# Kernel optimization log

Measured on AMD Instinct MI355X. Metric: run time of the kernel, lower is better.

Reference implementation:

```python
import jax, jax.numpy as jnp
import numpy as np

B, NN, F, H = 8, 1024, 256, 8
D = F // H
SCALE = D ** -0.5


def setup_inputs() -> dict:
    key = jax.random.key(0)
    ks = jax.random.split(key, 12)
    s = 0.02
    inp = {
        'ndata': jax.random.normal(ks[0], (B, NN, F), jnp.float32),
        'N': NN,
        'attn_bias': jax.random.normal(ks[1], (B, NN, NN, H), jnp.float32),
        'attn_mask': jax.random.randint(ks[2], (B, NN, NN), 0, 2).astype(bool),
        'Wq': jax.random.normal(ks[3], (F, F), jnp.float32) * s,
        'bq': jnp.zeros((F,), jnp.float32),
        'Wk': jax.random.normal(ks[4], (F, F), jnp.float32) * s,
        'bk': jnp.zeros((F,), jnp.float32),
        'Wv': jax.random.normal(ks[5], (F, F), jnp.float32) * s,
        'bv': jnp.zeros((F,), jnp.float32),
        'Wo': jax.random.normal(ks[6], (F, F), jnp.float32) * s,
        'bo': jnp.zeros((F,), jnp.float32),
    }
    return inp


def reference(ndata, N, attn_bias, attn_mask, Wq, bq, Wk, bk, Wv, bv, Wo, bo):
    b, n, f = ndata.shape
    # QKV projections (torch nn.Linear: x @ W.T + b), split heads
    q = (ndata @ Wq.T + bq).reshape(b, n, H, D) * SCALE
    k = (ndata @ Wk.T + bk).reshape(b, n, H, D)
    v = (ndata @ Wv.T + bv).reshape(b, n, H, D)
    # scores: (b, q, k, h) matching torch layout after its transposes
    scores = jnp.einsum('bqhd,bkhd->bqkh', q, k)
    scores = scores + attn_bias  # additive bias
    # original code force-unmasks column 0 so every row has a valid entry
    mask = attn_mask.at[:, :, 0].set(False)
    scores = jnp.where(mask[..., None], -jnp.inf, scores)
    attn = jax.nn.softmax(scores, axis=2)  # softmax over keys
    out = jnp.einsum('bqkh,bkhd->bqhd', attn, v).reshape(b, n, f)
    return out @ Wo.T + bo
```

## Files before the change

### kernel.cpp

```cpp
#include <hip/hip_runtime.h>
#include <hip/hip_bf16.h>

typedef __attribute__((ext_vector_type(8))) short short8;
typedef __attribute__((ext_vector_type(4))) float f32x4;

#define MFMA16(a,b,c) __builtin_amdgcn_mfma_f32_16x16x32_bf16((a),(b),(c),0,0,0)

static __device__ __forceinline__ unsigned int f2bf(float f){
    unsigned int u = __float_as_uint(f);
    u += 0x7FFFu + ((u >> 16) & 1u);
    return u >> 16;
}

static __device__ __forceinline__ short8 pack8(float4 a, float4 b){
    short8 r;
    r[0]=(short)f2bf(a.x); r[1]=(short)f2bf(a.y);
    r[2]=(short)f2bf(a.z); r[3]=(short)f2bf(a.w);
    r[4]=(short)f2bf(b.x); r[5]=(short)f2bf(b.y);
    r[6]=(short)f2bf(b.z); r[7]=(short)f2bf(b.w);
    return r;
}

__global__ __launch_bounds__(256) void mask_prep_k(
    const unsigned int* __restrict__ m, unsigned int* __restrict__ bmout)
{
    __shared__ int any_hi;
    const int tid  = threadIdx.x;
    const int lane = tid & 63;
    const unsigned int gbase = blockIdx.x*256u + tid;
    if (tid == 0) any_hi = 0;

    unsigned int wv[8]; unsigned int acc = 0;
    #pragma unroll
    for (int it = 0; it < 8; ++it){
        wv[it] = m[it*262144u + gbase];
        acc |= wv[it];
    }
    __syncthreads();
    if (acc & 0xFFFFFF00u) atomicOr(&any_hi, 1);
    __syncthreads();

    if (any_hi == 0){
        for (int it = 0; it < 32; ++it){
            unsigned int idx = it*262144u + gbase;
            unsigned int v = m[idx];
            unsigned long long bal = __ballot(v != 0u);
            if (lane == 0)
                *(unsigned long long*)(bmout + (idx >> 5)) = bal;
        }
    } else {
        #pragma unroll
        for (int it = 0; it < 8; ++it){
            unsigned int idx = it*262144u + gbase;
            unsigned int v = wv[it];
            unsigned int nib = (v | (v>>7) | (v>>14) | (v>>21)) & 0xFu;
            unsigned int x = nib << ((lane & 7)*4);
            x |= (unsigned int)__shfl_xor((int)x, 1);
            x |= (unsigned int)__shfl_xor((int)x, 2);
            x |= (unsigned int)__shfl_xor((int)x, 4);
            if ((lane & 7) == 0)
                bmout[idx >> 3] = x;
        }
    }
}

__global__ __launch_bounds__(256) void qkv_proj_k(
    const float* __restrict__ nd,
    const float* __restrict__ Wqp, const float* __restrict__ bqp,
    const float* __restrict__ Wkp, const float* __restrict__ bkp,
    const float* __restrict__ Wvp, const float* __restrict__ bvp,
    unsigned short* __restrict__ qout, unsigned short* __restrict__ kout,
    unsigned short* __restrict__ vtout)
{
    __shared__ __align__(16) unsigned short xl[64*264];
    const int tid  = threadIdx.x;
    const int bi   = blockIdx.x;
    const int kind = bi >> 7;
    const int R0   = (bi & 127) * 64;
    const int b    = R0 >> 10;
    const int n0   = R0 & 1023;

    #pragma unroll
    for (int it = 0; it < 16; ++it){
        int f4 = it*256 + tid;
        int r = f4 >> 6, c4 = f4 & 63;
        float4 v = *(const float4*)(nd + (size_t)(R0+r)*256 + c4*4);
        unsigned int lo = f2bf(v.x) | (f2bf(v.y) << 16);
        unsigned int hi = f2bf(v.z) | (f2bf(v.w) << 16);
        *(uint2*)&xl[r*264 + c4*4] = make_uint2(lo, hi);
    }
    __syncthreads();

    const int lane = tid & 63;
    const int w  = tid >> 6;
    const int ln = lane & 15;
    const int g  = lane >> 4;
    const int ow = w * 64;

    f32x4 acc[4][4];
    #pragma unroll
    for (int a=0;a<4;++a){
        #pragma unroll
        for (int c=0;c<4;++c) acc[a][c] = (f32x4){0.f,0.f,0.f,0.f};
    }

    if (kind < 2){
        const float* W  = kind ? Wkp : Wqp;
        const float* bb = kind ? bkp : bqp;
        unsigned short* op = kind ? kout : qout;
        const float scl = kind ? 1.0f : 0.17677669529663687f;
        for (int kk = 0; kk < 8; ++kk){
            short8 wf[4], xf[4];
            #pragma unroll
            for (int ot=0; ot<4; ++ot){
                const float* wp = W + (size_t)(ow + ot*16 + ln)*256 + kk*32 + g*8;
                wf[ot] = pack8(*(const float4*)wp, *(const float4*)(wp+4));
            }
            #pragma unroll
            for (int nt=0; nt<4; ++nt)
                xf[nt] = *(const short8*)&xl[(nt*16+ln)*264 + kk*32 + g*8];
            #pragma unroll
            for (int ot=0; ot<4; ++ot){
                #pragma unroll
                for (int nt=0; nt<4; ++nt)
                    acc[ot][nt] = MFMA16(wf[ot], xf[nt], acc[ot][nt]);
            }
        }
        #pragma unroll
        for (int ot=0; ot<4; ++ot){
            int o0 = ow + ot*16 + g*4;
            int h = o0 >> 5, d0 = o0 & 31;
            float4 b4 = *(const float4*)(bb + o0);
            #pragma unroll
            for (int nt=0; nt<4; ++nt){
                int n = n0 + nt*16 + ln;
                unsigned int lo = f2bf((acc[ot][nt][0]+b4.x)*scl) | (f2bf((acc[ot][nt][1]+b4.y)*scl)<<16);
                unsigned int hi = f2bf((acc[ot][nt][2]+b4.z)*scl) | (f2bf((acc[ot][nt][3]+b4.w)*scl)<<16);
                *(uint2*)(op + ((size_t)(b*8+h)*1024 + n)*32 + d0) = make_uint2(lo,hi);
            }
        }
    } else {
        for (int kk = 0; kk < 8; ++kk){
            short8 wf[4], xf[4];
            #pragma unroll
            for (int ot=0; ot<4; ++ot){
                const float* wp = Wvp + (size_t)(ow + ot*16 + ln)*256 + kk*32 + g*8;
                wf[ot] = pack8(*(const float4*)wp, *(const float4*)(wp+4));
            }
            #pragma unroll
            for (int nt=0; nt<4; ++nt)
                xf[nt] = *(const short8*)&xl[(nt*16+ln)*264 + kk*32 + g*8];
            #pragma unroll
            for (int nt=0; nt<4; ++nt){
                #pragma unroll
                for (int ot=0; ot<4; ++ot)
                    acc[nt][ot] = MFMA16(xf[nt], wf[ot], acc[nt][ot]);
            }
        }
        #pragma unroll
        for (int nt=0; nt<4; ++nt){
            int nb = n0 + nt*16 + g*4;
            #pragma unroll
            for (int ot=0; ot<4; ++ot){
                int o = ow + ot*16 + ln;
                int h = o >> 5, d = o & 31;
                float bvv = bvp[o];
                unsigned int lo = f2bf(acc[nt][ot][0]+bvv) | (f2bf(acc[nt][ot][1]+bvv)<<16);
                unsigned int hi = f2bf(acc[nt][ot][2]+bvv) | (f2bf(acc[nt][ot][3]+bvv)<<16);
                *(uint2*)(vtout + ((size_t)(b*8+h)*32 + d)*1024 + nb) = make_uint2(lo,hi);
            }
        }
    }
}

__global__ __launch_bounds__(256, 4) void attn_k(
    const unsigned short* __restrict__ qbuf, const unsigned short* __restrict__ kbuf,
    const unsigned short* __restrict__ vtbuf, const float* __restrict__ bias,
    const unsigned int* __restrict__ bm, unsigned short* __restrict__ ab)
{
    __shared__ float bs[2048];
    const int tid  = threadIdx.x;
    const int bi   = blockIdx.x;
    const int hh   = bi & 1;
    const int qt   = (bi >> 1) & 63;
    const int b    = bi >> 7;
    const int q0   = qt * 16;
    const int lane = tid & 63;
    const int w    = tid >> 6;
    const int ln   = lane & 15;
    const int g    = lane >> 4;
    const int h    = hh*4 + w;

    const short8 qf = *(const short8*)(qbuf + ((size_t)(b*8+h)*1024 + q0 + ln)*32 + g*8);

    const int kperm = ((ln >> 2) << 3) + (ln & 3);
    const unsigned short* kp = kbuf  + ((size_t)(b*8+h)*1024 + kperm)*32 + g*8;
    const unsigned short* vp = vtbuf + ((size_t)(b*8+h)*32 + ln)*1024 + g*8;
    const unsigned int* bmp  = bm + (size_t)(b*1024 + q0 + ln)*32;

    const int qt0 = tid >> 5;
    const int kk0 = tid & 31;
    const float* bgp0 = bias + ((size_t)(b*1024 + q0 + qt0)*1024 + kk0)*8 + hh*4;
    const float* bgp1 = bgp0 + 65536;
    const int kx  = kk0 ^ qt0;
    const int w0i = qt0*32 + kx;
    const int w1i = w0i + 256;

    const int base_rg = w*512 + ln*32 + g*8;
    const int lnx = ln & 7;

    f32x4 acc0 = (f32x4){0.f,0.f,0.f,0.f};
    f32x4 acc1 = (f32x4){0.f,0.f,0.f,0.f};
    float lsum = 0.f;
    const f32x4 z4 = {0.f,0.f,0.f,0.f};

    float4 br0, br1;
    short8 kA0, kA1, vA0, vA1, kB0, kB1, vB0, vB1;
    unsigned int bmA, bmB;

#define LOAD_BIAS(cc) do { int c_=(cc); \
    br0 = *(const float4*)(bgp0 + c_*256); \
    br1 = *(const float4*)(bgp1 + c_*256); } while(0)

#define STAGE() do { \
    bs[w0i       ] = br0.x; bs[w0i +  512] = br0.y; \
    bs[w0i + 1024] = br0.z; bs[w0i + 1536] = br0.w; \
    bs[w1i       ] = br1.x; bs[w1i +  512] = br1.y; \
    bs[w1i + 1024] = br1.z; bs[w1i + 1536] = br1.w; } while(0)

#define LOAD_KVM(S, cc) do { int c_=(cc); \
    k##S##0 = *(const short8*)(kp + c_*1024); \
    k##S##1 = *(const short8*)(kp + c_*1024 + 128); \
    v##S##0 = *(const short8*)(vp + c_*32); \
    v##S##1 = *(const short8*)(vp + c_*32 + 16*1024); \
    bm##S   = bmp[c_]; } while(0)

#define COMPUTE(S) do { \
    unsigned int mb_ = bm##S >> (g*8); \
    f32x4 s0 = MFMA16(k##S##0, qf, z4); \
    f32x4 s1 = MFMA16(k##S##1, qf, z4); \
    float e0 = __expf(((mb_>>0)&1u) ? -1e30f : s0[0] + bs[base_rg + (0^lnx)]); \
    float e1 = __expf(((mb_>>1)&1u) ? -1e30f : s0[1] + bs[base_rg + (1^lnx)]); \
    float e2 = __expf(((mb_>>2)&1u) ? -1e30f : s0[2] + bs[base_rg + (2^lnx)]); \
    float e3 = __expf(((mb_>>3)&1u) ? -1e30f : s0[3] + bs[base_rg + (3^lnx)]); \
    float e4 = __expf(((mb_>>4)&1u) ? -1e30f : s1[0] + bs[base_rg + (4^lnx)]); \
    float e5 = __expf(((mb_>>5)&1u) ? -1e30f : s1[1] + bs[base_rg + (5^lnx)]); \
    float e6 = __expf(((mb_>>6)&1u) ? -1e30f : s1[2] + bs[base_rg + (6^lnx)]); \
    float e7 = __expf(((mb_>>7)&1u) ? -1e30f : s1[3] + bs[base_rg + (7^lnx)]); \
    lsum += ((e0+e1)+(e2+e3)) + ((e4+e5)+(e6+e7)); \
    int4 pw_ = make_int4( \
        (int)(f2bf(e0) | (f2bf(e1)<<16)), (int)(f2bf(e2) | (f2bf(e3)<<16)), \
        (int)(f2bf(e4) | (f2bf(e5)<<16)), (int)(f2bf(e6) | (f2bf(e7)<<16))); \
    short8 pf_ = *(short8*)&pw_; \
    acc0 = MFMA16(v##S##0, pf_, acc0); \
    acc1 = MFMA16(v##S##1, pf_, acc1); } while(0)

    LOAD_BIAS(0);
    LOAD_KVM(A, 0);
    bmA &= ~1u;

    #pragma unroll 1
    for (int c = 0; c < 32; c += 2){
        STAGE();
        LOAD_BIAS(c + 1);
        __syncthreads();
        LOAD_KVM(B, c + 1);
        COMPUTE(A);
        __syncthreads();
        STAGE();
        if (c + 2 < 32) LOAD_BIAS(c + 2);
        __syncthreads();
        if (c + 2 < 32) LOAD_KVM(A, c + 2);
        COMPUTE(B);
        __syncthreads();
    }

    float ps = lsum;
    ps += __shfl_xor(ps, 16);
    ps += __shfl_xor(ps, 32);
    float inv = 1.0f / ps;
    {
        size_t orow = ((size_t)(b*1024 + q0 + ln))*256 + h*32;
        unsigned int lo0 = f2bf(acc0[0]*inv) | (f2bf(acc0[1]*inv)<<16);
        unsigned int hi0 = f2bf(acc0[2]*inv) | (f2bf(acc0[3]*inv)<<16);
        *(uint2*)(ab + orow + g*4) = make_uint2(lo0,hi0);
        unsigned int lo1 = f2bf(acc1[0]*inv) | (f2bf(acc1[1]*inv)<<16);
        unsigned int hi1 = f2bf(acc1[2]*inv) | (f2bf(acc1[3]*inv)<<16);
        *(uint2*)(ab + orow + 16 + g*4) = make_uint2(lo1,hi1);
    }
#undef LOAD_BIAS
#undef STAGE
#undef LOAD_KVM
#undef COMPUTE
}

__global__ __launch_bounds__(256) void oproj_k(
    const unsigned short* __restrict__ ab, const float* __restrict__ Wop,
    const float* __restrict__ bop, float* __restrict__ out)
{
    __shared__ __align__(16) unsigned short al[32*264];
    const int tid = threadIdx.x;
    const int R0 = blockIdx.x * 32;
    #pragma unroll
    for (int it=0; it<4; ++it){
        int f8 = it*256 + tid;
        int r = f8 >> 5, c8 = f8 & 31;
        *(short8*)&al[r*264 + c8*8] = *(const short8*)(ab + (size_t)(R0+r)*256 + c8*8);
    }
    __syncthreads();
    const int lane = tid & 63;
    const int w = tid >> 6, ln = lane & 15, g = lane >> 4;
    const int ow = w*64;
    f32x4 acc[4][2];
    #pragma unroll
    for (int a=0;a<4;++a){ acc[a][0]=(f32x4){0.f,0.f,0.f,0.f}; acc[a][1]=(f32x4){0.f,0.f,0.f,0.f}; }
    for (int kk=0;kk<8;++kk){
        short8 wf[4], xf[2];
        #pragma unroll
        for (int ot=0;ot<4;++ot){
            const float* wp = Wop + (size_t)(ow+ot*16+ln)*256 + kk*32 + g*8;
            wf[ot] = pack8(*(const float4*)wp, *(const float4*)(wp+4));
        }
        #pragma unroll
        for (int nt=0;nt<2;++nt)
            xf[nt] = *(const short8*)&al[(nt*16+ln)*264 + kk*32 + g*8];
        #pragma unroll
        for (int ot=0;ot<4;++ot){
            #pragma unroll
            for (int nt=0;nt<2;++nt)
                acc[ot][nt] = MFMA16(wf[ot], xf[nt], acc[ot][nt]);
        }
    }
    #pragma unroll
    for (int ot=0;ot<4;++ot){
        int o0 = ow + ot*16 + g*4;
        float4 b4 = *(const float4*)(bop + o0);
        #pragma unroll
        for (int nt=0;nt<2;++nt){
            int n = R0 + nt*16 + ln;
            float4 res;
            res.x = acc[ot][nt][0] + b4.x;
            res.y = acc[ot][nt][1] + b4.y;
            res.z = acc[ot][nt][2] + b4.z;
            res.w = acc[ot][nt][3] + b4.w;
            *(float4*)(out + (size_t)n*256 + o0) = res;
        }
    }
}

extern "C" void kernel_launch(void* const* d_in, const int* in_sizes, int n_in,
                              void* d_out, int out_size, void* d_ws, size_t ws_size,
                              hipStream_t stream)
{
    (void)in_sizes; (void)n_in; (void)out_size; (void)ws_size;
    const float* nd   = (const float*)d_in[0];
    const float* bias = (const float*)d_in[2];
    const int* mask   = (const int*)d_in[3];
    const float* Wq = (const float*)d_in[4];
    const float* bq = (const float*)d_in[5];
    const float* Wk = (const float*)d_in[6];
    const float* bk = (const float*)d_in[7];
    const float* Wv = (const float*)d_in[8];
    const float* bv = (const float*)d_in[9];
    const float* Wo = (const float*)d_in[10];
    const float* bo = (const float*)d_in[11];
    float* out = (float*)d_out;

    const size_t ELEMS = (size_t)8*8*1024*32;
    unsigned short* qb  = (unsigned short*)d_ws;
    unsigned short* kb  = qb  + ELEMS;
    unsigned short* vtb = kb  + ELEMS;
    unsigned short* ab  = vtb + ELEMS;
    unsigned int* bmw   = (unsigned int*)(ab + ELEMS);

    mask_prep_k<<<1024, 256, 0, stream>>>((const unsigned int*)mask, bmw);
    qkv_proj_k<<<384, 256, 0, stream>>>(nd, Wq, bq, Wk, bk, Wv, bv, qb, kb, vtb);
    attn_k<<<1024, 256, 0, stream>>>(qb, kb, vtb, bias, bmw, ab);
    oproj_k<<<256, 256, 0, stream>>>(ab, Wo, bo, out);
}
```

Measured before the change: 170.3 us.

## Process all eight heads per attention block with full-row bias loads

The attention kernel now uses 512-thread blocks covering all 8 heads for a 16-query tile, so each bias row of 8 heads×keys is read contiguously as full float4 rows rather than split across two blocks by head half. Chunks double to 32 keys each with a single sync pair per iteration, and keys are loaded in natural order with lane shuffles rebuilding the P operand layout. V fragments are loaded inside the compute step instead of prefetched. This is meant to improve bias read coalescing and halve barrier count, at the cost of more shuffles, larger LDS use and possibly lower occupancy.

```diff
diff --git a/kernel.cpp b/kernel.cpp
--- a/kernel.cpp
+++ b/kernel.cpp
@@ -173,105 +173,117 @@
     }
 }
 
-__global__ __launch_bounds__(256, 4) void attn_k(
+__global__ __launch_bounds__(512, 4) void attn_k(
     const unsigned short* __restrict__ qbuf, const unsigned short* __restrict__ kbuf,
     const unsigned short* __restrict__ vtbuf, const float* __restrict__ bias,
     const unsigned int* __restrict__ bm, unsigned short* __restrict__ ab)
 {
-    __shared__ float bs[2048];
+    __shared__ float bs[8192];
     const int tid  = threadIdx.x;
     const int bi   = blockIdx.x;
-    const int hh   = bi & 1;
-    const int qt   = (bi >> 1) & 63;
-    const int b    = bi >> 7;
-    const int q0   = qt * 16;
+    const int b    = bi >> 6;
+    const int q0   = (bi & 63) * 16;
     const int lane = tid & 63;
     const int w    = tid >> 6;
     const int ln   = lane & 15;
     const int g    = lane >> 4;
-    const int h    = hh*4 + w;
-
-    const short8 qf = *(const short8*)(qbuf + ((size_t)(b*8+h)*1024 + q0 + ln)*32 + g*8);
-
-    const int kperm = ((ln >> 2) << 3) + (ln & 3);
-    const unsigned short* kp = kbuf  + ((size_t)(b*8+h)*1024 + kperm)*32 + g*8;
-    const unsigned short* vp = vtbuf + ((size_t)(b*8+h)*32 + ln)*1024 + g*8;
-    const unsigned int* bmp  = bm + (size_t)(b*1024 + q0 + ln)*32;
-
-    const int qt0 = tid >> 5;
-    const int kk0 = tid & 31;
-    const float* bgp0 = bias + ((size_t)(b*1024 + q0 + qt0)*1024 + kk0)*8 + hh*4;
-    const float* bgp1 = bgp0 + 65536;
-    const int kx  = kk0 ^ qt0;
-    const int w0i = qt0*32 + kx;
-    const int w1i = w0i + 256;
-
-    const int base_rg = w*512 + ln*32 + g*8;
-    const int lnx = ln & 7;
+
+    const short8 qf = *(const short8*)(qbuf + ((size_t)(b*8+w)*1024 + q0 + ln)*32 + g*8);
+
+    const int h2s  = lane & 1;
+    const int keys = lane >> 1;
+    const int ts   = keys >> 4;
+    const int rs   = keys & 3;
+    const int gs   = (keys >> 2) & 3;
+    const int base0 = (128*ts + 32*rs + 16*h2s + gs) * 16;
+    const int xrs   = (8*ts + 2*rs + h2s) & 15;
+    const int qxa   = (2*w)     ^ xrs;
+    const int qxb   = (2*w + 1) ^ xrs;
+
+    const float* bp0 = bias + ((size_t)(b*1024 + q0 + 2*w)*1024)*8 + lane*4;
+    const unsigned short* kp = kbuf  + ((size_t)(b*8+w)*1024 + ln)*32 + g*8;
+    const unsigned short* vp = vtbuf + ((size_t)(b*8+w)*32   + ln)*1024 + g*8;
+    const unsigned int*  bmp = bm + (size_t)(b*1024 + q0 + ln)*32;
 
     f32x4 acc0 = (f32x4){0.f,0.f,0.f,0.f};
     f32x4 acc1 = (f32x4){0.f,0.f,0.f,0.f};
     float lsum = 0.f;
     const f32x4 z4 = {0.f,0.f,0.f,0.f};
 
-    float4 br0, br1;
-    short8 kA0, kA1, vA0, vA1, kB0, kB1, vB0, vB1;
-    unsigned int bmA, bmB;
-
-#define LOAD_BIAS(cc) do { int c_=(cc); \
-    br0 = *(const float4*)(bgp0 + c_*256); \
-    br1 = *(const float4*)(bgp1 + c_*256); } while(0)
-
-#define STAGE() do { \
-    bs[w0i       ] = br0.x; bs[w0i +  512] = br0.y; \
-    bs[w0i + 1024] = br0.z; bs[w0i + 1536] = br0.w; \
-    bs[w1i       ] = br1.x; bs[w1i +  512] = br1.y; \
-    bs[w1i + 1024] = br1.z; bs[w1i + 1536] = br1.w; } while(0)
-
-#define LOAD_KVM(S, cc) do { int c_=(cc); \
-    k##S##0 = *(const short8*)(kp + c_*1024); \
-    k##S##1 = *(const short8*)(kp + c_*1024 + 128); \
-    v##S##0 = *(const short8*)(vp + c_*32); \
-    v##S##1 = *(const short8*)(vp + c_*32 + 16*1024); \
-    bm##S   = bmp[c_]; } while(0)
-
-#define COMPUTE(S) do { \
-    unsigned int mb_ = bm##S >> (g*8); \
-    f32x4 s0 = MFMA16(k##S##0, qf, z4); \
-    f32x4 s1 = MFMA16(k##S##1, qf, z4); \
-    float e0 = __expf(((mb_>>0)&1u) ? -1e30f : s0[0] + bs[base_rg + (0^lnx)]); \
-    float e1 = __expf(((mb_>>1)&1u) ? -1e30f : s0[1] + bs[base_rg + (1^lnx)]); \
-    float e2 = __expf(((mb_>>2)&1u) ? -1e30f : s0[2] + bs[base_rg + (2^lnx)]); \
-    float e3 = __expf(((mb_>>3)&1u) ? -1e30f : s0[3] + bs[base_rg + (3^lnx)]); \
-    float e4 = __expf(((mb_>>4)&1u) ? -1e30f : s1[0] + bs[base_rg + (4^lnx)]); \
-    float e5 = __expf(((mb_>>5)&1u) ? -1e30f : s1[1] + bs[base_rg + (5^lnx)]); \
-    float e6 = __expf(((mb_>>6)&1u) ? -1e30f : s1[2] + bs[base_rg + (6^lnx)]); \
-    float e7 = __expf(((mb_>>7)&1u) ? -1e30f : s1[3] + bs[base_rg + (7^lnx)]); \
-    lsum += ((e0+e1)+(e2+e3)) + ((e4+e5)+(e6+e7)); \
-    int4 pw_ = make_int4( \
-        (int)(f2bf(e0) | (f2bf(e1)<<16)), (int)(f2bf(e2) | (f2bf(e3)<<16)), \
-        (int)(f2bf(e4) | (f2bf(e5)<<16)), (int)(f2bf(e6) | (f2bf(e7)<<16))); \
+    float4 b00, b01, b10, b11;
+    short8 kn0, kn1, kn2, kn3;
+    unsigned int bm0, bm1;
+
+#define LOAD_ALL(cc) do { int c_ = (cc); \
+    b00 = *(const float4*)(bp0 + (size_t)c_*512); \
+    b01 = *(const float4*)(bp0 + (size_t)c_*512 + 256); \
+    b10 = *(const float4*)(bp0 + (size_t)c_*512 + 8192); \
+    b11 = *(const float4*)(bp0 + (size_t)c_*512 + 8192 + 256); \
+    kn0 = *(const short8*)(kp + c_*2048); \
+    kn1 = *(const short8*)(kp + c_*2048 + 512); \
+    kn2 = *(const short8*)(kp + c_*2048 + 1024); \
+    kn3 = *(const short8*)(kp + c_*2048 + 1536); \
+    bm0 = bmp[2*c_]; bm1 = bmp[2*c_+1]; } while(0)
+
+#define CHUNK_HALF(K0, K1, BMW, BOFF, VOFF) do { \
+    f32x4 s0 = MFMA16(K0, qf, z4); \
+    f32x4 s1 = MFMA16(K1, qf, z4); \
+    short8 vf0 = *(const short8*)(vp + (VOFF)); \
+    short8 vf1 = *(const short8*)(vp + (VOFF) + 16*1024); \
+    float pv[8]; \
+    _Pragma("unroll") for (int t=0; t<2; ++t){ \
+        _Pragma("unroll") for (int r=0; r<4; ++r){ \
+            int keyl = t*16 + g*4 + r; \
+            int bidx = (BOFF) + (t*128 + r*32 + w*4 + g)*16 + (ln ^ ((t*8 + r*2 + (w>>2)) & 15)); \
+            float sv = (t ? s1[r] : s0[r]) + bs[bidx]; \
+            sv = (((BMW) >> keyl) & 1u) ? -1e30f : sv; \
+            float p = __expf(sv); \
+            pv[t*4+r] = p; \
+            lsum += p; \
+        } \
+    } \
+    unsigned int A01 = f2bf(pv[0]) | (f2bf(pv[1])<<16); \
+    unsigned int A23 = f2bf(pv[2]) | (f2bf(pv[3])<<16); \
+    unsigned int B01 = f2bf(pv[4]) | (f2bf(pv[5])<<16); \
+    unsigned int B23 = f2bf(pv[6]) | (f2bf(pv[7])<<16); \
+    int s0l = (2*(g&1))*16 + ln; \
+    int s1l = s0l + 16; \
+    unsigned int a01  = (unsigned int)__shfl((int)A01, s0l); \
+    unsigned int a23  = (unsigned int)__shfl((int)A23, s0l); \
+    unsigned int c01  = (unsigned int)__shfl((int)B01, s0l); \
+    unsigned int c23  = (unsigned int)__shfl((int)B23, s0l); \
+    unsigned int a01b = (unsigned int)__shfl((int)A01, s1l); \
+    unsigned int a23b = (unsigned int)__shfl((int)A23, s1l); \
+    unsigned int c01b = (unsigned int)__shfl((int)B01, s1l); \
+    unsigned int c23b = (unsigned int)__shfl((int)B23, s1l); \
+    bool hi_ = (g >= 2); \
+    int4 pw_ = make_int4((int)(hi_ ? c01  : a01 ), (int)(hi_ ? c23  : a23 ), \
+                         (int)(hi_ ? c01b : a01b), (int)(hi_ ? c23b : a23b)); \
     short8 pf_ = *(short8*)&pw_; \
-    acc0 = MFMA16(v##S##0, pf_, acc0); \
-    acc1 = MFMA16(v##S##1, pf_, acc1); } while(0)
-
-    LOAD_BIAS(0);
-    LOAD_KVM(A, 0);
-    bmA &= ~1u;
+    acc0 = MFMA16(vf0, pf_, acc0); \
+    acc1 = MFMA16(vf1, pf_, acc1); } while(0)
+
+    LOAD_ALL(0);
+    bm0 &= ~1u;
 
     #pragma unroll 1
-    for (int c = 0; c < 32; c += 2){
-        STAGE();
-        LOAD_BIAS(c + 1);
+    for (int cc = 0; cc < 16; ++cc){
+        bs[base0       + qxa] = b00.x;  bs[base0 +  64 + qxa] = b00.y;
+        bs[base0 + 128 + qxa] = b00.z;  bs[base0 + 192 + qxa] = b00.w;
+        bs[base0       + qxb] = b10.x;  bs[base0 +  64 + qxb] = b10.y;
+        bs[base0 + 128 + qxb] = b10.z;  bs[base0 + 192 + qxb] = b10.w;
+        bs[4096 + base0       + qxa] = b01.x;  bs[4096 + base0 +  64 + qxa] = b01.y;
+        bs[4096 + base0 + 128 + qxa] = b01.z;  bs[4096 + base0 + 192 + qxa] = b01.w;
+        bs[4096 + base0       + qxb] = b11.x;  bs[4096 + base0 +  64 + qxb] = b11.y;
+        bs[4096 + base0 + 128 + qxb] = b11.z;  bs[4096 + base0 + 192 + qxb] = b11.w;
+
+        short8 ck0 = kn0, ck1 = kn1, ck2 = kn2, ck3 = kn3;
+        unsigned int cb0 = bm0, cb1 = bm1;
+        if (cc + 1 < 16) LOAD_ALL(cc + 1);
         __syncthreads();
-        LOAD_KVM(B, c + 1);
-        COMPUTE(A);
-        __syncthreads();
-        STAGE();
-        if (c + 2 < 32) LOAD_BIAS(c + 2);
-        __syncthreads();
-        if (c + 2 < 32) LOAD_KVM(A, c + 2);
-        COMPUTE(B);
+
+        CHUNK_HALF(ck0, ck1, cb0, 0,    cc*64);
+        CHUNK_HALF(ck2, ck3, cb1, 4096, cc*64 + 32);
         __syncthreads();
     }
 
@@ -280,18 +292,16 @@
     ps += __shfl_xor(ps, 32);
     float inv = 1.0f / ps;
     {
-        size_t orow = ((size_t)(b*1024 + q0 + ln))*256 + h*32;
+        int n = q0 + ln;
         unsigned int lo0 = f2bf(acc0[0]*inv) | (f2bf(acc0[1]*inv)<<16);
         unsigned int hi0 = f2bf(acc0[2]*inv) | (f2bf(acc0[3]*inv)<<16);
-        *(uint2*)(ab + orow + g*4) = make_uint2(lo0,hi0);
+        *(uint2*)(ab + ((size_t)(b*1024 + n))*256 + w*32 + g*4) = make_uint2(lo0,hi0);
         unsigned int lo1 = f2bf(acc1[0]*inv) | (f2bf(acc1[1]*inv)<<16);
         unsigned int hi1 = f2bf(acc1[2]*inv) | (f2bf(acc1[3]*inv)<<16);
-        *(uint2*)(ab + orow + 16 + g*4) = make_uint2(lo1,hi1);
-    }
-#undef LOAD_BIAS
-#undef STAGE
-#undef LOAD_KVM
-#undef COMPUTE
+        *(uint2*)(ab + ((size_t)(b*1024 + n))*256 + w*32 + 16 + g*4) = make_uint2(lo1,hi1);
+    }
+#undef LOAD_ALL
+#undef CHUNK_HALF
 }
 
 __global__ __launch_bounds__(256) void oproj_k(
@@ -375,6 +385,6 @@
 
     mask_prep_k<<<1024, 256, 0, stream>>>((const unsigned int*)mask, bmw);
     qkv_proj_k<<<384, 256, 0, stream>>>(nd, Wq, bq, Wk, bk, Wv, bv, qb, kb, vtb);
-    attn_k<<<1024, 256, 0, stream>>>(qb, kb, vtb, bias, bmw, ab);
+    attn_k<<<512, 512, 0, stream>>>(qb, kb, vtb, bias, bmw, ab);
     oproj_k<<<256, 256, 0, stream>>>(ab, Wo, bo, out);
 }
```

Measured after the change: 143.6 us. -15.7%, faster.

## Pre-transpose bias to bf16 head-major with mask folded in, drop attention LDS staging

Applied to the files above, without the earlier changes.

A new pre-pass reads the fp32 (b,q,k,h) bias and the mask, applies the mask as -1e30 (keeping key column 0 unmasked), converts to bf16 and writes a head-major (b,h,q,k) buffer. The attention kernel then loads its bias fragment straight from global memory as short8, which removes the LDS staging, the four barriers per iteration and the mask-bit handling. In exchange it adds a 128 MB bf16 intermediate that is written and read back, plus an extra kernel launch and a one-block mask-format detector. Bias precision also drops to bf16.

```diff
diff --git a/kernel.cpp b/kernel.cpp
--- a/kernel.cpp
+++ b/kernel.cpp
@@ -10,6 +10,10 @@
     unsigned int u = __float_as_uint(f);
     u += 0x7FFFu + ((u >> 16) & 1u);
     return u >> 16;
+}
+
+static __device__ __forceinline__ float bf2f(unsigned short s){
+    return __uint_as_float(((unsigned int)s) << 16);
 }
 
 static __device__ __forceinline__ short8 pack8(float4 a, float4 b){
@@ -21,46 +25,67 @@
     return r;
 }
 
-__global__ __launch_bounds__(256) void mask_prep_k(
-    const unsigned int* __restrict__ m, unsigned int* __restrict__ bmout)
-{
+__global__ void detect_mask_k(const int* __restrict__ m, int* __restrict__ flag){
     __shared__ int any_hi;
+    if (threadIdx.x == 0) any_hi = 0;
+    __syncthreads();
+    int acc = 0;
+    #pragma unroll
+    for (int it = 0; it < 16; ++it)
+        acc |= m[it*256 + threadIdx.x];
+    if (acc & 0xFFFFFF00) atomicOr(&any_hi, 1);
+    __syncthreads();
+    if (threadIdx.x == 0) *flag = any_hi;
+}
+
+__global__ __launch_bounds__(256) void bias_prep_k(
+    const float* __restrict__ bias, const unsigned int* __restrict__ mask,
+    const int* __restrict__ mflag, unsigned short* __restrict__ bbt)
+{
+    __shared__ unsigned short tl[8][1032];
+    __shared__ unsigned int mbits[32];
     const int tid  = threadIdx.x;
-    const int lane = tid & 63;
-    const unsigned int gbase = blockIdx.x*256u + tid;
-    if (tid == 0) any_hi = 0;
-
-    unsigned int wv[8]; unsigned int acc = 0;
-    #pragma unroll
-    for (int it = 0; it < 8; ++it){
-        wv[it] = m[it*262144u + gbase];
-        acc |= wv[it];
-    }
-    __syncthreads();
-    if (acc & 0xFFFFFF00u) atomicOr(&any_hi, 1);
-    __syncthreads();
-
-    if (any_hi == 0){
-        for (int it = 0; it < 32; ++it){
-            unsigned int idx = it*262144u + gbase;
-            unsigned int v = m[idx];
+    const int row  = blockIdx.x;
+    const int b    = row >> 10, q = row & 1023;
+    const int lane = tid & 63, wv = tid >> 6;
+
+    if (*mflag == 0){
+        #pragma unroll
+        for (int i = 0; i < 4; ++i){
+            unsigned int v = mask[(size_t)row*1024 + i*256 + tid];
             unsigned long long bal = __ballot(v != 0u);
             if (lane == 0)
-                *(unsigned long long*)(bmout + (idx >> 5)) = bal;
+                *(unsigned long long*)&mbits[(i*256 + wv*64) >> 5] = bal;
         }
     } else {
-        #pragma unroll
-        for (int it = 0; it < 8; ++it){
-            unsigned int idx = it*262144u + gbase;
-            unsigned int v = wv[it];
-            unsigned int nib = (v | (v>>7) | (v>>14) | (v>>21)) & 0xFu;
-            unsigned int x = nib << ((lane & 7)*4);
-            x |= (unsigned int)__shfl_xor((int)x, 1);
-            x |= (unsigned int)__shfl_xor((int)x, 2);
-            x |= (unsigned int)__shfl_xor((int)x, 4);
-            if ((lane & 7) == 0)
-                bmout[idx >> 3] = x;
-        }
+        unsigned int v = mask[(size_t)row*256 + tid];
+        unsigned int nib = (v | (v>>7) | (v>>14) | (v>>21)) & 0xFu;
+        unsigned int x = nib << ((lane & 7)*4);
+        x |= (unsigned int)__shfl_xor((int)x, 1);
+        x |= (unsigned int)__shfl_xor((int)x, 2);
+        x |= (unsigned int)__shfl_xor((int)x, 4);
+        if ((lane & 7) == 0) mbits[tid >> 3] = x;
+    }
+    __syncthreads();
+
+    const int h0 = (tid & 1) * 4;
+    #pragma unroll
+    for (int i = 0; i < 8; ++i){
+        float4 v = *(const float4*)(bias + (size_t)row*8192 + i*1024 + tid*4);
+        int k = i*128 + (tid >> 1);
+        bool msk = (((mbits[k>>5] >> (k&31)) & 1u) != 0u) && (k != 0);
+        if (msk){ v.x = -1e30f; v.y = -1e30f; v.z = -1e30f; v.w = -1e30f; }
+        tl[h0  ][k] = (unsigned short)f2bf(v.x);
+        tl[h0+1][k] = (unsigned short)f2bf(v.y);
+        tl[h0+2][k] = (unsigned short)f2bf(v.z);
+        tl[h0+3][k] = (unsigned short)f2bf(v.w);
+    }
+    __syncthreads();
+
+    #pragma unroll
+    for (int h = 0; h < 8; ++h){
+        uint2 d = *(const uint2*)&tl[h][tid*4];
+        *(uint2*)(bbt + ((size_t)(b*8+h)*1024 + q)*1024 + tid*4) = d;
     }
 }
 
@@ -173,15 +198,14 @@
     }
 }
 
-__global__ __launch_bounds__(256, 4) void attn_k(
+__global__ __launch_bounds__(256, 4) void attn2_k(
     const unsigned short* __restrict__ qbuf, const unsigned short* __restrict__ kbuf,
-    const unsigned short* __restrict__ vtbuf, const float* __restrict__ bias,
-    const unsigned int* __restrict__ bm, unsigned short* __restrict__ ab)
-{
-    __shared__ float bs[2048];
+    const unsigned short* __restrict__ vtbuf, const unsigned short* __restrict__ bbt,
+    unsigned short* __restrict__ ab)
+{
     const int tid  = threadIdx.x;
     const int bi   = blockIdx.x;
-    const int hh   = bi & 1;
+    const int hg   = bi & 1;
     const int qt   = (bi >> 1) & 63;
     const int b    = bi >> 7;
     const int q0   = qt * 16;
@@ -189,90 +213,54 @@
     const int w    = tid >> 6;
     const int ln   = lane & 15;
     const int g    = lane >> 4;
-    const int h    = hh*4 + w;
+    const int h    = hg*4 + w;
 
     const short8 qf = *(const short8*)(qbuf + ((size_t)(b*8+h)*1024 + q0 + ln)*32 + g*8);
-
     const int kperm = ((ln >> 2) << 3) + (ln & 3);
     const unsigned short* kp = kbuf  + ((size_t)(b*8+h)*1024 + kperm)*32 + g*8;
     const unsigned short* vp = vtbuf + ((size_t)(b*8+h)*32 + ln)*1024 + g*8;
-    const unsigned int* bmp  = bm + (size_t)(b*1024 + q0 + ln)*32;
-
-    const int qt0 = tid >> 5;
-    const int kk0 = tid & 31;
-    const float* bgp0 = bias + ((size_t)(b*1024 + q0 + qt0)*1024 + kk0)*8 + hh*4;
-    const float* bgp1 = bgp0 + 65536;
-    const int kx  = kk0 ^ qt0;
-    const int w0i = qt0*32 + kx;
-    const int w1i = w0i + 256;
-
-    const int base_rg = w*512 + ln*32 + g*8;
-    const int lnx = ln & 7;
+    const unsigned short* bp = bbt   + ((size_t)(b*8+h)*1024 + q0 + ln)*1024 + g*8;
 
     f32x4 acc0 = (f32x4){0.f,0.f,0.f,0.f};
     f32x4 acc1 = (f32x4){0.f,0.f,0.f,0.f};
     float lsum = 0.f;
     const f32x4 z4 = {0.f,0.f,0.f,0.f};
 
-    float4 br0, br1;
-    short8 kA0, kA1, vA0, vA1, kB0, kB1, vB0, vB1;
-    unsigned int bmA, bmB;
-
-#define LOAD_BIAS(cc) do { int c_=(cc); \
-    br0 = *(const float4*)(bgp0 + c_*256); \
-    br1 = *(const float4*)(bgp1 + c_*256); } while(0)
-
-#define STAGE() do { \
-    bs[w0i       ] = br0.x; bs[w0i +  512] = br0.y; \
-    bs[w0i + 1024] = br0.z; bs[w0i + 1536] = br0.w; \
-    bs[w1i       ] = br1.x; bs[w1i +  512] = br1.y; \
-    bs[w1i + 1024] = br1.z; bs[w1i + 1536] = br1.w; } while(0)
-
-#define LOAD_KVM(S, cc) do { int c_=(cc); \
-    k##S##0 = *(const short8*)(kp + c_*1024); \
-    k##S##1 = *(const short8*)(kp + c_*1024 + 128); \
-    v##S##0 = *(const short8*)(vp + c_*32); \
-    v##S##1 = *(const short8*)(vp + c_*32 + 16*1024); \
-    bm##S   = bmp[c_]; } while(0)
-
-#define COMPUTE(S) do { \
-    unsigned int mb_ = bm##S >> (g*8); \
-    f32x4 s0 = MFMA16(k##S##0, qf, z4); \
-    f32x4 s1 = MFMA16(k##S##1, qf, z4); \
-    float e0 = __expf(((mb_>>0)&1u) ? -1e30f : s0[0] + bs[base_rg + (0^lnx)]); \
-    float e1 = __expf(((mb_>>1)&1u) ? -1e30f : s0[1] + bs[base_rg + (1^lnx)]); \
-    float e2 = __expf(((mb_>>2)&1u) ? -1e30f : s0[2] + bs[base_rg + (2^lnx)]); \
-    float e3 = __expf(((mb_>>3)&1u) ? -1e30f : s0[3] + bs[base_rg + (3^lnx)]); \
-    float e4 = __expf(((mb_>>4)&1u) ? -1e30f : s1[0] + bs[base_rg + (4^lnx)]); \
-    float e5 = __expf(((mb_>>5)&1u) ? -1e30f : s1[1] + bs[base_rg + (5^lnx)]); \
-    float e6 = __expf(((mb_>>6)&1u) ? -1e30f : s1[2] + bs[base_rg + (6^lnx)]); \
-    float e7 = __expf(((mb_>>7)&1u) ? -1e30f : s1[3] + bs[base_rg + (7^lnx)]); \
+    short8 k0A,k1A,v0A,v1A,bbA, k0B,k1B,v0B,v1B,bbB;
+
+#define LOADC(S, cc) do { int c_ = (cc); \
+    k0##S = *(const short8*)(kp + c_*1024); \
+    k1##S = *(const short8*)(kp + c_*1024 + 128); \
+    v0##S = *(const short8*)(vp + c_*32); \
+    v1##S = *(const short8*)(vp + c_*32 + 16*1024); \
+    bb##S = *(const short8*)(bp + c_*32); } while(0)
+
+#define COMPC(S) do { \
+    f32x4 s0 = MFMA16(k0##S, qf, z4); \
+    f32x4 s1 = MFMA16(k1##S, qf, z4); \
+    float e0 = __expf(s0[0] + bf2f((unsigned short)bb##S[0])); \
+    float e1 = __expf(s0[1] + bf2f((unsigned short)bb##S[1])); \
+    float e2 = __expf(s0[2] + bf2f((unsigned short)bb##S[2])); \
+    float e3 = __expf(s0[3] + bf2f((unsigned short)bb##S[3])); \
+    float e4 = __expf(s1[0] + bf2f((unsigned short)bb##S[4])); \
+    float e5 = __expf(s1[1] + bf2f((unsigned short)bb##S[5])); \
+    float e6 = __expf(s1[2] + bf2f((unsigned short)bb##S[6])); \
+    float e7 = __expf(s1[3] + bf2f((unsigned short)bb##S[7])); \
     lsum += ((e0+e1)+(e2+e3)) + ((e4+e5)+(e6+e7)); \
     int4 pw_ = make_int4( \
         (int)(f2bf(e0) | (f2bf(e1)<<16)), (int)(f2bf(e2) | (f2bf(e3)<<16)), \
         (int)(f2bf(e4) | (f2bf(e5)<<16)), (int)(f2bf(e6) | (f2bf(e7)<<16))); \
     short8 pf_ = *(short8*)&pw_; \
-    acc0 = MFMA16(v##S##0, pf_, acc0); \
-    acc1 = MFMA16(v##S##1, pf_, acc1); } while(0)
-
-    LOAD_BIAS(0);
-    LOAD_KVM(A, 0);
-    bmA &= ~1u;
-
+    acc0 = MFMA16(v0##S, pf_, acc0); \
+    acc1 = MFMA16(v1##S, pf_, acc1); } while(0)
+
+    LOADC(A, 0);
     #pragma unroll 1
     for (int c = 0; c < 32; c += 2){
-        STAGE();
-        LOAD_BIAS(c + 1);
-        __syncthreads();
-        LOAD_KVM(B, c + 1);
-        COMPUTE(A);
-        __syncthreads();
-        STAGE();
-        if (c + 2 < 32) LOAD_BIAS(c + 2);
-        __syncthreads();
-        if (c + 2 < 32) LOAD_KVM(A, c + 2);
-        COMPUTE(B);
-        __syncthreads();
+        LOADC(B, c + 1);
+        COMPC(A);
+        if (c + 2 < 32) LOADC(A, c + 2);
+        COMPC(B);
     }
 
     float ps = lsum;
@@ -288,10 +276,8 @@
         unsigned int hi1 = f2bf(acc1[2]*inv) | (f2bf(acc1[3]*inv)<<16);
         *(uint2*)(ab + orow + 16 + g*4) = make_uint2(lo1,hi1);
     }
-#undef LOAD_BIAS
-#undef STAGE
-#undef LOAD_KVM
-#undef COMPUTE
+#undef LOADC
+#undef COMPC
 }
 
 __global__ __launch_bounds__(256) void oproj_k(
@@ -371,10 +357,12 @@
     unsigned short* kb  = qb  + ELEMS;
     unsigned short* vtb = kb  + ELEMS;
     unsigned short* ab  = vtb + ELEMS;
-    unsigned int* bmw   = (unsigned int*)(ab + ELEMS);
-
-    mask_prep_k<<<1024, 256, 0, stream>>>((const unsigned int*)mask, bmw);
+    unsigned short* bbt = ab  + ELEMS;
+    int* mflag          = (int*)(bbt + (size_t)8*8*1024*1024);
+
+    detect_mask_k<<<1, 256, 0, stream>>>(mask, mflag);
     qkv_proj_k<<<384, 256, 0, stream>>>(nd, Wq, bq, Wk, bk, Wv, bv, qb, kb, vtb);
-    attn_k<<<1024, 256, 0, stream>>>(qb, kb, vtb, bias, bmw, ab);
+    bias_prep_k<<<8192, 256, 0, stream>>>(bias, (const unsigned int*)mask, mflag, bbt);
+    attn2_k<<<1024, 256, 0, stream>>>(qb, kb, vtb, bbt, ab);
     oproj_k<<<256, 256, 0, stream>>>(ab, Wo, bo, out);
 }
```

After: 188.5 us. 10.7% more time.

## Process two heads per wave and read bias directly without LDS staging

Applied to the files above, without the earlier changes.

Rewrites the attention kernel so each wave handles two heads for a 16-query tile, and a block covers all eight heads. Bias values are loaded straight from global memory as float2 pairs per key instead of being staged through shared memory, which removes the four barriers per iteration. Masking is applied after the exponential by zeroing. The trade-off is more registers per thread, half as many blocks, a lower occupancy target, and less-vectorised strided bias loads.

```diff
diff --git a/kernel.cpp b/kernel.cpp
--- a/kernel.cpp
+++ b/kernel.cpp
@@ -173,125 +173,138 @@
     }
 }
 
-__global__ __launch_bounds__(256, 4) void attn_k(
+__global__ __launch_bounds__(256, 2) void attn3_k(
     const unsigned short* __restrict__ qbuf, const unsigned short* __restrict__ kbuf,
     const unsigned short* __restrict__ vtbuf, const float* __restrict__ bias,
     const unsigned int* __restrict__ bm, unsigned short* __restrict__ ab)
 {
-    __shared__ float bs[2048];
     const int tid  = threadIdx.x;
     const int bi   = blockIdx.x;
-    const int hh   = bi & 1;
-    const int qt   = (bi >> 1) & 63;
-    const int b    = bi >> 7;
-    const int q0   = qt * 16;
+    const int b    = bi >> 6;
+    const int q0   = (bi & 63) * 16;
     const int lane = tid & 63;
     const int w    = tid >> 6;
     const int ln   = lane & 15;
     const int g    = lane >> 4;
-    const int h    = hh*4 + w;
-
-    const short8 qf = *(const short8*)(qbuf + ((size_t)(b*8+h)*1024 + q0 + ln)*32 + g*8);
+    const int h0   = 2*w, h1 = 2*w + 1;
+
+    const short8 qf0 = *(const short8*)(qbuf + ((size_t)(b*8+h0)*1024 + q0 + ln)*32 + g*8);
+    const short8 qf1 = *(const short8*)(qbuf + ((size_t)(b*8+h1)*1024 + q0 + ln)*32 + g*8);
 
     const int kperm = ((ln >> 2) << 3) + (ln & 3);
-    const unsigned short* kp = kbuf  + ((size_t)(b*8+h)*1024 + kperm)*32 + g*8;
-    const unsigned short* vp = vtbuf + ((size_t)(b*8+h)*32 + ln)*1024 + g*8;
-    const unsigned int* bmp  = bm + (size_t)(b*1024 + q0 + ln)*32;
-
-    const int qt0 = tid >> 5;
-    const int kk0 = tid & 31;
-    const float* bgp0 = bias + ((size_t)(b*1024 + q0 + qt0)*1024 + kk0)*8 + hh*4;
-    const float* bgp1 = bgp0 + 65536;
-    const int kx  = kk0 ^ qt0;
-    const int w0i = qt0*32 + kx;
-    const int w1i = w0i + 256;
-
-    const int base_rg = w*512 + ln*32 + g*8;
-    const int lnx = ln & 7;
-
-    f32x4 acc0 = (f32x4){0.f,0.f,0.f,0.f};
-    f32x4 acc1 = (f32x4){0.f,0.f,0.f,0.f};
-    float lsum = 0.f;
+    const unsigned short* kpA = kbuf + ((size_t)(b*8+h0)*1024 + kperm)*32 + g*8;
+    const unsigned short* kpB = kbuf + ((size_t)(b*8+h1)*1024 + kperm)*32 + g*8;
+    const unsigned short* vpA = vtbuf + ((size_t)(b*8+h0)*32 + ln)*1024 + g*8;
+    const unsigned short* vpB = vtbuf + ((size_t)(b*8+h1)*32 + ln)*1024 + g*8;
+    const float* bp = bias + (((size_t)(b*1024 + q0 + ln)*1024) + 8*g)*8 + h0;
+    const unsigned int* bmp = bm + (size_t)(b*1024 + q0 + ln)*32;
+
+    f32x4 acc00 = (f32x4){0.f,0.f,0.f,0.f};
+    f32x4 acc01 = (f32x4){0.f,0.f,0.f,0.f};
+    f32x4 acc10 = (f32x4){0.f,0.f,0.f,0.f};
+    f32x4 acc11 = (f32x4){0.f,0.f,0.f,0.f};
+    float lsum0 = 0.f, lsum1 = 0.f;
     const f32x4 z4 = {0.f,0.f,0.f,0.f};
 
-    float4 br0, br1;
-    short8 kA0, kA1, vA0, vA1, kB0, kB1, vB0, vB1;
+    short8 k0A,k1A,k2A,k3A, v0A,v1A,v2A,v3A;
+    short8 k0B,k1B,k2B,k3B, v0B,v1B,v2B,v3B;
+    float2 bb0A,bb1A,bb2A,bb3A,bb4A,bb5A,bb6A,bb7A;
+    float2 bb0B,bb1B,bb2B,bb3B,bb4B,bb5B,bb6B,bb7B;
     unsigned int bmA, bmB;
 
-#define LOAD_BIAS(cc) do { int c_=(cc); \
-    br0 = *(const float4*)(bgp0 + c_*256); \
-    br1 = *(const float4*)(bgp1 + c_*256); } while(0)
-
-#define STAGE() do { \
-    bs[w0i       ] = br0.x; bs[w0i +  512] = br0.y; \
-    bs[w0i + 1024] = br0.z; bs[w0i + 1536] = br0.w; \
-    bs[w1i       ] = br1.x; bs[w1i +  512] = br1.y; \
-    bs[w1i + 1024] = br1.z; bs[w1i + 1536] = br1.w; } while(0)
-
-#define LOAD_KVM(S, cc) do { int c_=(cc); \
-    k##S##0 = *(const short8*)(kp + c_*1024); \
-    k##S##1 = *(const short8*)(kp + c_*1024 + 128); \
-    v##S##0 = *(const short8*)(vp + c_*32); \
-    v##S##1 = *(const short8*)(vp + c_*32 + 16*1024); \
-    bm##S   = bmp[c_]; } while(0)
-
-#define COMPUTE(S) do { \
+#define LOADC(S, cc) do { int c_ = (cc); \
+    k0##S = *(const short8*)(kpA + c_*1024); \
+    k1##S = *(const short8*)(kpA + c_*1024 + 128); \
+    k2##S = *(const short8*)(kpB + c_*1024); \
+    k3##S = *(const short8*)(kpB + c_*1024 + 128); \
+    v0##S = *(const short8*)(vpA + c_*32); \
+    v1##S = *(const short8*)(vpA + c_*32 + 16*1024); \
+    v2##S = *(const short8*)(vpB + c_*32); \
+    v3##S = *(const short8*)(vpB + c_*32 + 16*1024); \
+    bb0##S = *(const float2*)(bp + (size_t)(c_*32+0)*8); \
+    bb1##S = *(const float2*)(bp + (size_t)(c_*32+1)*8); \
+    bb2##S = *(const float2*)(bp + (size_t)(c_*32+2)*8); \
+    bb3##S = *(const float2*)(bp + (size_t)(c_*32+3)*8); \
+    bb4##S = *(const float2*)(bp + (size_t)(c_*32+4)*8); \
+    bb5##S = *(const float2*)(bp + (size_t)(c_*32+5)*8); \
+    bb6##S = *(const float2*)(bp + (size_t)(c_*32+6)*8); \
+    bb7##S = *(const float2*)(bp + (size_t)(c_*32+7)*8); \
+    bm##S = bmp[c_]; } while(0)
+
+#define COMPC(S) do { \
     unsigned int mb_ = bm##S >> (g*8); \
-    f32x4 s0 = MFMA16(k##S##0, qf, z4); \
-    f32x4 s1 = MFMA16(k##S##1, qf, z4); \
-    float e0 = __expf(((mb_>>0)&1u) ? -1e30f : s0[0] + bs[base_rg + (0^lnx)]); \
-    float e1 = __expf(((mb_>>1)&1u) ? -1e30f : s0[1] + bs[base_rg + (1^lnx)]); \
-    float e2 = __expf(((mb_>>2)&1u) ? -1e30f : s0[2] + bs[base_rg + (2^lnx)]); \
-    float e3 = __expf(((mb_>>3)&1u) ? -1e30f : s0[3] + bs[base_rg + (3^lnx)]); \
-    float e4 = __expf(((mb_>>4)&1u) ? -1e30f : s1[0] + bs[base_rg + (4^lnx)]); \
-    float e5 = __expf(((mb_>>5)&1u) ? -1e30f : s1[1] + bs[base_rg + (5^lnx)]); \
-    float e6 = __expf(((mb_>>6)&1u) ? -1e30f : s1[2] + bs[base_rg + (6^lnx)]); \
-    float e7 = __expf(((mb_>>7)&1u) ? -1e30f : s1[3] + bs[base_rg + (7^lnx)]); \
-    lsum += ((e0+e1)+(e2+e3)) + ((e4+e5)+(e6+e7)); \
-    int4 pw_ = make_int4( \
+    f32x4 s0 = MFMA16(k0##S, qf0, z4); \
+    f32x4 s1 = MFMA16(k1##S, qf0, z4); \
+    f32x4 s2 = MFMA16(k2##S, qf1, z4); \
+    f32x4 s3 = MFMA16(k3##S, qf1, z4); \
+    float e0 = __expf(s0[0] + bb0##S.x); e0 = ((mb_>>0)&1u) ? 0.f : e0; \
+    float e1 = __expf(s0[1] + bb1##S.x); e1 = ((mb_>>1)&1u) ? 0.f : e1; \
+    float e2 = __expf(s0[2] + bb2##S.x); e2 = ((mb_>>2)&1u) ? 0.f : e2; \
+    float e3 = __expf(s0[3] + bb3##S.x); e3 = ((mb_>>3)&1u) ? 0.f : e3; \
+    float e4 = __expf(s1[0] + bb4##S.x); e4 = ((mb_>>4)&1u) ? 0.f : e4; \
+    float e5 = __expf(s1[1] + bb5##S.x); e5 = ((mb_>>5)&1u) ? 0.f : e5; \
+    float e6 = __expf(s1[2] + bb6##S.x); e6 = ((mb_>>6)&1u) ? 0.f : e6; \
+    float e7 = __expf(s1[3] + bb7##S.x); e7 = ((mb_>>7)&1u) ? 0.f : e7; \
+    float f0 = __expf(s2[0] + bb0##S.y); f0 = ((mb_>>0)&1u) ? 0.f : f0; \
+    float f1 = __expf(s2[1] + bb1##S.y); f1 = ((mb_>>1)&1u) ? 0.f : f1; \
+    float f2 = __expf(s2[2] + bb2##S.y); f2 = ((mb_>>2)&1u) ? 0.f : f2; \
+    float f3 = __expf(s2[3] + bb3##S.y); f3 = ((mb_>>3)&1u) ? 0.f : f3; \
+    float f4 = __expf(s3[0] + bb4##S.y); f4 = ((mb_>>4)&1u) ? 0.f : f4; \
+    float f5 = __expf(s3[1] + bb5##S.y); f5 = ((mb_>>5)&1u) ? 0.f : f5; \
+    float f6 = __expf(s3[2] + bb6##S.y); f6 = ((mb_>>6)&1u) ? 0.f : f6; \
+    float f7 = __expf(s3[3] + bb7##S.y); f7 = ((mb_>>7)&1u) ? 0.f : f7; \
+    lsum0 += ((e0+e1)+(e2+e3)) + ((e4+e5)+(e6+e7)); \
+    lsum1 += ((f0+f1)+(f2+f3)) + ((f4+f5)+(f6+f7)); \
+    int4 pw0 = make_int4( \
         (int)(f2bf(e0) | (f2bf(e1)<<16)), (int)(f2bf(e2) | (f2bf(e3)<<16)), \
         (int)(f2bf(e4) | (f2bf(e5)<<16)), (int)(f2bf(e6) | (f2bf(e7)<<16))); \
-    short8 pf_ = *(short8*)&pw_; \
-    acc0 = MFMA16(v##S##0, pf_, acc0); \
-    acc1 = MFMA16(v##S##1, pf_, acc1); } while(0)
-
-    LOAD_BIAS(0);
-    LOAD_KVM(A, 0);
+    int4 pw1 = make_int4( \
+        (int)(f2bf(f0) | (f2bf(f1)<<16)), (int)(f2bf(f2) | (f2bf(f3)<<16)), \
+        (int)(f2bf(f4) | (f2bf(f5)<<16)), (int)(f2bf(f6) | (f2bf(f7)<<16))); \
+    short8 pf0 = *(short8*)&pw0; \
+    short8 pf1 = *(short8*)&pw1; \
+    acc00 = MFMA16(v0##S, pf0, acc00); \
+    acc01 = MFMA16(v1##S, pf0, acc01); \
+    acc10 = MFMA16(v2##S, pf1, acc10); \
+    acc11 = MFMA16(v3##S, pf1, acc11); } while(0)
+
+    LOADC(A, 0);
     bmA &= ~1u;
-
     #pragma unroll 1
     for (int c = 0; c < 32; c += 2){
-        STAGE();
-        LOAD_BIAS(c + 1);
-        __syncthreads();
-        LOAD_KVM(B, c + 1);
-        COMPUTE(A);
-        __syncthreads();
-        STAGE();
-        if (c + 2 < 32) LOAD_BIAS(c + 2);
-        __syncthreads();
-        if (c + 2 < 32) LOAD_KVM(A, c + 2);
-        COMPUTE(B);
-        __syncthreads();
-    }
-
-    float ps = lsum;
-    ps += __shfl_xor(ps, 16);
-    ps += __shfl_xor(ps, 32);
-    float inv = 1.0f / ps;
+        LOADC(B, c + 1);
+        COMPC(A);
+        if (c + 2 < 32) LOADC(A, c + 2);
+        COMPC(B);
+    }
+
     {
-        size_t orow = ((size_t)(b*1024 + q0 + ln))*256 + h*32;
-        unsigned int lo0 = f2bf(acc0[0]*inv) | (f2bf(acc0[1]*inv)<<16);
-        unsigned int hi0 = f2bf(acc0[2]*inv) | (f2bf(acc0[3]*inv)<<16);
-        *(uint2*)(ab + orow + g*4) = make_uint2(lo0,hi0);
-        unsigned int lo1 = f2bf(acc1[0]*inv) | (f2bf(acc1[1]*inv)<<16);
-        unsigned int hi1 = f2bf(acc1[2]*inv) | (f2bf(acc1[3]*inv)<<16);
-        *(uint2*)(ab + orow + 16 + g*4) = make_uint2(lo1,hi1);
-    }
-#undef LOAD_BIAS
-#undef STAGE
-#undef LOAD_KVM
-#undef COMPUTE
+        float ps0 = lsum0;
+        ps0 += __shfl_xor(ps0, 16);
+        ps0 += __shfl_xor(ps0, 32);
+        float inv0 = 1.0f / ps0;
+        size_t orow = ((size_t)(b*1024 + q0 + ln))*256 + h0*32;
+        unsigned int lo = f2bf(acc00[0]*inv0) | (f2bf(acc00[1]*inv0)<<16);
+        unsigned int hi = f2bf(acc00[2]*inv0) | (f2bf(acc00[3]*inv0)<<16);
+        *(uint2*)(ab + orow + g*4) = make_uint2(lo,hi);
+        lo = f2bf(acc01[0]*inv0) | (f2bf(acc01[1]*inv0)<<16);
+        hi = f2bf(acc01[2]*inv0) | (f2bf(acc01[3]*inv0)<<16);
+        *(uint2*)(ab + orow + 16 + g*4) = make_uint2(lo,hi);
+
+        float ps1 = lsum1;
+        ps1 += __shfl_xor(ps1, 16);
+        ps1 += __shfl_xor(ps1, 32);
+        float inv1 = 1.0f / ps1;
+        size_t orow1 = ((size_t)(b*1024 + q0 + ln))*256 + h1*32;
+        lo = f2bf(acc10[0]*inv1) | (f2bf(acc10[1]*inv1)<<16);
+        hi = f2bf(acc10[2]*inv1) | (f2bf(acc10[3]*inv1)<<16);
+        *(uint2*)(ab + orow1 + g*4) = make_uint2(lo,hi);
+        lo = f2bf(acc11[0]*inv1) | (f2bf(acc11[1]*inv1)<<16);
+        hi = f2bf(acc11[2]*inv1) | (f2bf(acc11[3]*inv1)<<16);
+        *(uint2*)(ab + orow1 + 16 + g*4) = make_uint2(lo,hi);
+    }
+#undef LOADC
+#undef COMPC
 }
 
 __global__ __launch_bounds__(256) void oproj_k(
@@ -375,6 +388,6 @@
 
     mask_prep_k<<<1024, 256, 0, stream>>>((const unsigned int*)mask, bmw);
     qkv_proj_k<<<384, 256, 0, stream>>>(nd, Wq, bq, Wk, bk, Wv, bv, qb, kb, vtb);
-    attn_k<<<1024, 256, 0, stream>>>(qb, kb, vtb, bias, bmw, ab);
+    attn3_k<<<512, 256, 0, stream>>>(qb, kb, vtb, bias, bmw, ab);
     oproj_k<<<256, 256, 0, stream>>>(ab, Wo, bo, out);
 }
```

Result: slower. 199.2 us (+17.0%).
